# Kernel optimization log

Hardware: AMD Instinct MI355X
Metric: run time of the kernel (lower is better)

Reference implementation:

```python
import jax, jax.numpy as jnp
import numpy as np
from jax import lax

N = 100000      # number of nodes (== ninput)
E = 3200000     # number of edges per adjacency
NHID = 128
EPS = 1e-12     # torch F.normalize eps


def spmm(src, dst, w, x):
    # sparse adj @ x : out[i] = sum_{e: dst[e]==i} w[e] * x[src[e]]
    return jax.ops.segment_sum(w[:, None] * x[src], dst, num_segments=N)


def l2norm(x):
    # F.normalize(x, p=2, dim=1)
    n = jnp.sqrt(jnp.sum(x * x, axis=1, keepdims=True))
    return x / jnp.maximum(n, EPS)


def mlp(x, L1, bl1, L2, bl2, L3, bl3):
    # dropout == 0.0 -> identity; chunking is a memory optimization, same math
    h = jax.nn.relu(x @ L1 + bl1)
    h = jax.nn.relu(h @ L2 + bl2)
    return h @ L3 + bl3  # [N, 1]


def setup_inputs() -> dict:
    key = jax.random.key(0)
    ks = jax.random.split(key, 32)
    d = {}
    d["adj1_src"] = jax.random.randint(ks[0], (E,), 0, N, dtype=jnp.int32)
    d["adj1_dst"] = jax.random.randint(ks[1], (E,), 0, N, dtype=jnp.int32)
    d["adj1_w"] = jax.random.uniform(ks[2], (E,), dtype=jnp.float32)
    d["adj2_src"] = jax.random.randint(ks[3], (E,), 0, N, dtype=jnp.int32)
    d["adj2_dst"] = jax.random.randint(ks[4], (E,), 0, N, dtype=jnp.int32)
    d["adj2_w"] = jax.random.uniform(ks[5], (E,), dtype=jnp.float32)
    d["W1"] = jax.random.normal(ks[6], (N, NHID), dtype=jnp.float32) * 0.05
    d["b1"] = jnp.zeros((NHID,), jnp.float32)
    for i, k in zip(range(2, 7), ks[7:12]):
        d[f"W{i}"] = jax.random.normal(k, (NHID, NHID), dtype=jnp.float32) * (1.0 / np.sqrt(NHID))
        d[f"b{i}"] = jnp.zeros((NHID,), jnp.float32)
    d["L1"] = jax.random.normal(ks[12], (NHID, 2 * NHID), dtype=jnp.float32) * (1.0 / np.sqrt(NHID))
    d["bl1"] = jnp.zeros((2 * NHID,), jnp.float32)
    d["L2"] = jax.random.normal(ks[13], (2 * NHID, 2 * NHID), dtype=jnp.float32) * (1.0 / np.sqrt(2 * NHID))
    d["bl2"] = jnp.zeros((2 * NHID,), jnp.float32)
    d["L3"] = jax.random.normal(ks[14], (2 * NHID, 1), dtype=jnp.float32) * (1.0 / np.sqrt(2 * NHID))
    d["bl3"] = jnp.zeros((1,), jnp.float32)
    return d


def reference(adj1_src, adj1_dst, adj1_w, adj2_src, adj2_dst, adj2_w,
              W1, b1, W2, b2, W3, b3, W4, b4, W5, b5, W6, b6,
              L1, bl1, L2, bl2, L3, bl3):
    def branch(src, dst, w):
        x1 = l2norm(jax.nn.relu(spmm(src, dst, w, W1) + b1))
        x2 = l2norm(jax.nn.relu(spmm(src, dst, w, x1 @ W2) + b2))
        x3 = l2norm(jax.nn.relu(spmm(src, dst, w, x2 @ W3) + b3))
        x4 = l2norm(jax.nn.relu(spmm(src, dst, w, x3 @ W4) + b4))
        x5 = l2norm(jax.nn.relu(spmm(src, dst, w, x4 @ W5) + b5))
        x6 = jax.nn.relu(spmm(src, dst, w, x5 @ W6) + b6)
        x7 = lax.stop_gradient(x1 + x2 + x3 + x4 + x5 + x6)  # .detach()
        s = jnp.zeros((N, 1), jnp.float32)
        for xi in (x1, x2, x3, x4, x5):  # computed under torch.no_grad()
            s = s + lax.stop_gradient(mlp(xi, L1, bl1, L2, bl2, L3, bl3))
        s = s + mlp(x6, L1, bl1, L2, bl2, L3, bl3)
        s = s + mlp(x7, L1, bl1, L2, bl2, L3, bl3)
        return s / 7.0

    score1 = branch(adj1_src, adj1_dst, adj1_w)
    score2 = branch(adj2_src, adj2_dst, adj2_w)
    return score1 * score2
```

## Files before the change

### kernel.cpp

```cpp
#include <hip/hip_runtime.h>

#define NN 100000
#define NE 3200000
#define HID 128
#define NNH ((size_t)NN * HID)
#define CAPB 80

typedef __attribute__((ext_vector_type(8))) _Float16 f16x8;
typedef __attribute__((ext_vector_type(4))) _Float16 f16x4;
typedef __attribute__((ext_vector_type(4))) float f32x4;

#define SWZ(row, k) ((k) ^ (((row) & 7) << 3))

__global__ void zero_k(int* p, int n) {
    int i = blockIdx.x * 256 + threadIdx.x;
    if (i < n) p[i] = 0;
}

__global__ void scatter_bin_k(const int* __restrict__ src, const int* __restrict__ dst,
                              const float* __restrict__ w, int* __restrict__ cnt,
                              unsigned* __restrict__ ep) {
    int e = blockIdx.x * 256 + threadIdx.x;
    if (e < NE) {
        int d = dst[e];
        int pos = atomicAdd(&cnt[d], 1);
        if (pos < CAPB) {
            ushort hb = __builtin_bit_cast(ushort, (_Float16)w[e]);
            ep[(size_t)d * CAPB + pos] = ((unsigned)src[e] << 15) | (unsigned)hb;
        }
    }
}

__global__ void convT_k(const float* __restrict__ W, _Float16* __restrict__ WT, int K, int N) {
    int idx = blockIdx.x * 256 + threadIdx.x;
    if (idx < K * N) {
        int k = idx / N, n = idx % N;
        WT[n * K + k] = (_Float16)W[idx];
    }
}

__global__ void conv4_k(const float* __restrict__ A, _Float16* __restrict__ B, int n4) {
    int i = blockIdx.x * 256 + threadIdx.x;
    if (i < n4) {
        float4 v = ((const float4*)A)[i];
        f16x4 h;
        h.x = (_Float16)v.x; h.y = (_Float16)v.y; h.z = (_Float16)v.z; h.w = (_Float16)v.w;
        ((f16x4*)B)[i] = h;
    }
}

template <bool EPI>
__global__ void spmm_k(const _Float16* __restrict__ x, const int* __restrict__ cnt,
                       const unsigned* __restrict__ ep, const float* __restrict__ bias,
                       _Float16* __restrict__ outx) {
    int row = blockIdx.x * 4 + (threadIdx.x >> 6);
    int l = threadIdx.x & 63;
    int q = l >> 4, li = l & 15;
    if (row >= NN) return;
    int e0 = row * CAPB;
    int deg = cnt[row];
    if (deg > CAPB) deg = CAPB;
    int e1 = e0 + deg;
    float acc[8] = {};
#pragma unroll 4
    for (int e = e0 + q; e < e1; e += 4) {
        unsigned r = ep[e];
        int s = r >> 15;
        float w = (float)__builtin_bit_cast(_Float16, (ushort)(r & 0x7FFFu));
        f16x8 v = *(const f16x8*)(x + (size_t)s * HID + li * 8);
#pragma unroll
        for (int j = 0; j < 8; ++j) acc[j] += w * (float)v[j];
    }
#pragma unroll
    for (int j = 0; j < 8; ++j) {
        acc[j] += __shfl_xor(acc[j], 16, 64);
        acc[j] += __shfl_xor(acc[j], 32, 64);
    }
    if (EPI) {
        const float4* bp = (const float4*)(bias + li * 8);
        float4 b0 = bp[0], b1 = bp[1];
        acc[0] = fmaxf(acc[0] + b0.x, 0.f); acc[1] = fmaxf(acc[1] + b0.y, 0.f);
        acc[2] = fmaxf(acc[2] + b0.z, 0.f); acc[3] = fmaxf(acc[3] + b0.w, 0.f);
        acc[4] = fmaxf(acc[4] + b1.x, 0.f); acc[5] = fmaxf(acc[5] + b1.y, 0.f);
        acc[6] = fmaxf(acc[6] + b1.z, 0.f); acc[7] = fmaxf(acc[7] + b1.w, 0.f);
        float ss = 0.f;
#pragma unroll
        for (int j = 0; j < 8; ++j) ss += acc[j] * acc[j];
        ss += __shfl_xor(ss, 1, 64);
        ss += __shfl_xor(ss, 2, 64);
        ss += __shfl_xor(ss, 4, 64);
        ss += __shfl_xor(ss, 8, 64);
        float sc = 1.0f / fmaxf(sqrtf(ss), 1e-12f);
#pragma unroll
        for (int j = 0; j < 8; ++j) acc[j] *= sc;
    }
    if (q == 0) {
        f16x8 ho;
#pragma unroll
        for (int j = 0; j < 8; ++j) ho[j] = (_Float16)acc[j];
        *(f16x8*)(outx + (size_t)row * HID + li * 8) = ho;
    }
}

template <bool NORM>
__global__ __launch_bounds__(256) void trans_mlp_k(
    const _Float16* __restrict__ Y, const _Float16* __restrict__ WT,
    const float* __restrict__ bw, _Float16* __restrict__ Xo,
    const _Float16* __restrict__ L1T, const float* __restrict__ bl1,
    const _Float16* __restrict__ L2T, const float* __restrict__ bl2,
    const float* __restrict__ L3, const float* __restrict__ bl3,
    float* __restrict__ sacc) {
    __shared__ _Float16 Xs[64][128];
    __shared__ _Float16 H1s[64][256];
    __shared__ float red[4][64];
    int t = threadIdx.x;
    int w = t >> 6, l = t & 63;
    int g = l >> 4, li = l & 15;
    int rowBase = blockIdx.x * 64;

#pragma unroll
    for (int i = 0; i < 4; ++i) {
        int idx = t + i * 256;
        int r = idx >> 4, c8 = idx & 15;
        int gr = rowBase + r;
        f16x8 v = (gr < NN) ? *(const f16x8*)(Y + (size_t)gr * 128 + c8 * 8)
                            : (f16x8)(_Float16)0.f;
        *(f16x8*)&Xs[r][SWZ(r, c8 * 8)] = v;
    }
    __syncthreads();

    int cW = w * 32;
    f32x4 accw[4][2] = {};
#pragma unroll
    for (int ks = 0; ks < 4; ++ks) {
        int kb = ks * 32 + g * 8;
        f16x8 a[4];
#pragma unroll
        for (int mt = 0; mt < 4; ++mt) {
            int r = mt * 16 + li;
            a[mt] = *(const f16x8*)&Xs[r][SWZ(r, kb)];
        }
#pragma unroll
        for (int nt = 0; nt < 2; ++nt) {
            f16x8 b = *(const f16x8*)(WT + (size_t)(cW + nt * 16 + li) * 128 + kb);
#pragma unroll
            for (int mt = 0; mt < 4; ++mt)
                accw[mt][nt] = __builtin_amdgcn_mfma_f32_16x16x32_f16(a[mt], b, accw[mt][nt], 0, 0, 0);
        }
    }
    float vv[4][2][4];
    float b0 = bw[cW + li], b1v = bw[cW + 16 + li];
#pragma unroll
    for (int mt = 0; mt < 4; ++mt)
#pragma unroll
        for (int r4 = 0; r4 < 4; ++r4) {
            vv[mt][0][r4] = fmaxf(accw[mt][0][r4] + b0, 0.f);
            vv[mt][1][r4] = fmaxf(accw[mt][1][r4] + b1v, 0.f);
        }
    if (NORM) {
#pragma unroll
        for (int mt = 0; mt < 4; ++mt)
#pragma unroll
            for (int r4 = 0; r4 < 4; ++r4) {
                float ps = vv[mt][0][r4] * vv[mt][0][r4] + vv[mt][1][r4] * vv[mt][1][r4];
                ps += __shfl_xor(ps, 1, 64);
                ps += __shfl_xor(ps, 2, 64);
                ps += __shfl_xor(ps, 4, 64);
                ps += __shfl_xor(ps, 8, 64);
                if (li == 0) red[w][mt * 16 + g * 4 + r4] = ps;
            }
        __syncthreads();
        if (t < 64) {
            float s = red[0][t] + red[1][t] + red[2][t] + red[3][t];
            red[0][t] = 1.f / fmaxf(sqrtf(s), 1e-12f);
        }
        __syncthreads();
    } else {
        __syncthreads();
    }
#pragma unroll
    for (int mt = 0; mt < 4; ++mt)
#pragma unroll
        for (int r4 = 0; r4 < 4; ++r4) {
            int row = mt * 16 + g * 4 + r4;
            float sc = NORM ? red[0][row] : 1.f;
            _Float16 h0 = (_Float16)(vv[mt][0][r4] * sc);
            _Float16 h1 = (_Float16)(vv[mt][1][r4] * sc);
            Xs[row][SWZ(row, cW + li)] = h0;
            Xs[row][SWZ(row, cW + 16 + li)] = h1;
            int gr = rowBase + row;
            if (gr < NN) {
                Xo[(size_t)gr * 128 + cW + li] = h0;
                Xo[(size_t)gr * 128 + cW + 16 + li] = h1;
            }
        }
    __syncthreads();

    int cM = w * 64;
    f32x4 acc[4][4] = {};
#pragma unroll
    for (int ks = 0; ks < 4; ++ks) {
        int kb = ks * 32 + g * 8;
        f16x8 a[4];
#pragma unroll
        for (int mt = 0; mt < 4; ++mt) {
            int r = mt * 16 + li;
            a[mt] = *(const f16x8*)&Xs[r][SWZ(r, kb)];
        }
#pragma unroll
        for (int nt = 0; nt < 4; ++nt) {
            int n = cM + nt * 16 + li;
            f16x8 b = *(const f16x8*)(L1T + (size_t)n * 128 + kb);
#pragma unroll
            for (int mt = 0; mt < 4; ++mt)
                acc[mt][nt] = __builtin_amdgcn_mfma_f32_16x16x32_f16(a[mt], b, acc[mt][nt], 0, 0, 0);
        }
    }
#pragma unroll
    for (int nt = 0; nt < 4; ++nt) {
        int col = cM + nt * 16 + li;
        float bb = bl1[col];
#pragma unroll
        for (int mt = 0; mt < 4; ++mt)
#pragma unroll
            for (int r4 = 0; r4 < 4; ++r4) {
                int row = mt * 16 + g * 4 + r4;
                H1s[row][SWZ(row, col)] = (_Float16)fmaxf(acc[mt][nt][r4] + bb, 0.f);
            }
    }
    __syncthreads();

    f32x4 acc2[4][4] = {};
#pragma unroll
    for (int ks = 0; ks < 8; ++ks) {
        int kb = ks * 32 + g * 8;
        f16x8 a[4];
#pragma unroll
        for (int mt = 0; mt < 4; ++mt) {
            int r = mt * 16 + li;
            a[mt] = *(const f16x8*)&H1s[r][SWZ(r, kb)];
        }
#pragma unroll
        for (int nt = 0; nt < 4; ++nt) {
            int n = cM + nt * 16 + li;
            f16x8 b = *(const f16x8*)(L2T + (size_t)n * 256 + kb);
#pragma unroll
            for (int mt = 0; mt < 4; ++mt)
                acc2[mt][nt] = __builtin_amdgcn_mfma_f32_16x16x32_f16(a[mt], b, acc2[mt][nt], 0, 0, 0);
        }
    }
    float part[4][4] = {};
#pragma unroll
    for (int nt = 0; nt < 4; ++nt) {
        int col = cM + nt * 16 + li;
        float bb = bl2[col];
        float l3v = L3[col];
#pragma unroll
        for (int mt = 0; mt < 4; ++mt)
#pragma unroll
            for (int r4 = 0; r4 < 4; ++r4)
                part[mt][r4] += fmaxf(acc2[mt][nt][r4] + bb, 0.f) * l3v;
    }
#pragma unroll
    for (int mt = 0; mt < 4; ++mt)
#pragma unroll
        for (int r4 = 0; r4 < 4; ++r4) {
            float p = part[mt][r4];
            p += __shfl_xor(p, 1, 64);
            p += __shfl_xor(p, 2, 64);
            p += __shfl_xor(p, 4, 64);
            p += __shfl_xor(p, 8, 64);
            if (li == 0) red[w][mt * 16 + g * 4 + r4] = p;
        }
    __syncthreads();
    if (t < 64) {
        int gr = rowBase + t;
        if (gr < NN)
            sacc[gr] += red[0][t] + red[1][t] + red[2][t] + red[3][t] + bl3[0];
    }
}

template <bool SUM6, bool INIT>
__global__ __launch_bounds__(256) void mlp_fused_k(
    const _Float16* __restrict__ X,
    const _Float16* __restrict__ L1T, const float* __restrict__ bl1,
    const _Float16* __restrict__ L2T, const float* __restrict__ bl2,
    const float* __restrict__ L3, const float* __restrict__ bl3,
    float* __restrict__ sacc) {
    __shared__ _Float16 Xs[64][128];
    __shared__ _Float16 H1s[64][256];
    __shared__ float red[4][64];
    int t = threadIdx.x;
    int w = t >> 6, l = t & 63;
    int g = l >> 4, li = l & 15;
    int rowBase = blockIdx.x * 64;

#pragma unroll
    for (int i = 0; i < 4; ++i) {
        int idx = t + i * 256;
        int r = idx >> 4, c8 = idx & 15;
        int gr = rowBase + r;
        if (SUM6) {
            float s[8] = {};
            if (gr < NN) {
#pragma unroll
                for (int l6 = 0; l6 < 6; ++l6) {
                    f16x8 v = *(const f16x8*)(X + (size_t)l6 * NNH + (size_t)gr * HID + c8 * 8);
#pragma unroll
                    for (int j = 0; j < 8; ++j) s[j] += (float)v[j];
                }
            }
            f16x8 hv;
#pragma unroll
            for (int j = 0; j < 8; ++j) hv[j] = (_Float16)s[j];
            *(f16x8*)&Xs[r][SWZ(r, c8 * 8)] = hv;
        } else {
            f16x8 v = (gr < NN) ? *(const f16x8*)(X + (size_t)gr * HID + c8 * 8)
                                : (f16x8)(_Float16)0.f;
            *(f16x8*)&Xs[r][SWZ(r, c8 * 8)] = v;
        }
    }
    __syncthreads();

    int cM = w * 64;
    f32x4 acc[4][4] = {};
#pragma unroll
    for (int ks = 0; ks < 4; ++ks) {
        int kb = ks * 32 + g * 8;
        f16x8 a[4];
#pragma unroll
        for (int mt = 0; mt < 4; ++mt) {
            int r = mt * 16 + li;
            a[mt] = *(const f16x8*)&Xs[r][SWZ(r, kb)];
        }
#pragma unroll
        for (int nt = 0; nt < 4; ++nt) {
            int n = cM + nt * 16 + li;
            f16x8 b = *(const f16x8*)(L1T + (size_t)n * 128 + kb);
#pragma unroll
            for (int mt = 0; mt < 4; ++mt)
                acc[mt][nt] = __builtin_amdgcn_mfma_f32_16x16x32_f16(a[mt], b, acc[mt][nt], 0, 0, 0);
        }
    }
#pragma unroll
    for (int nt = 0; nt < 4; ++nt) {
        int col = cM + nt * 16 + li;
        float bb = bl1[col];
#pragma unroll
        for (int mt = 0; mt < 4; ++mt)
#pragma unroll
            for (int r4 = 0; r4 < 4; ++r4) {
                int row = mt * 16 + g * 4 + r4;
                H1s[row][SWZ(row, col)] = (_Float16)fmaxf(acc[mt][nt][r4] + bb, 0.f);
            }
    }
    __syncthreads();

    f32x4 acc2[4][4] = {};
#pragma unroll
    for (int ks = 0; ks < 8; ++ks) {
        int kb = ks * 32 + g * 8;
        f16x8 a[4];
#pragma unroll
        for (int mt = 0; mt < 4; ++mt) {
            int r = mt * 16 + li;
            a[mt] = *(const f16x8*)&H1s[r][SWZ(r, kb)];
        }
#pragma unroll
        for (int nt = 0; nt < 4; ++nt) {
            int n = cM + nt * 16 + li;
            f16x8 b = *(const f16x8*)(L2T + (size_t)n * 256 + kb);
#pragma unroll
            for (int mt = 0; mt < 4; ++mt)
                acc2[mt][nt] = __builtin_amdgcn_mfma_f32_16x16x32_f16(a[mt], b, acc2[mt][nt], 0, 0, 0);
        }
    }
    float part[4][4] = {};
#pragma unroll
    for (int nt = 0; nt < 4; ++nt) {
        int col = cM + nt * 16 + li;
        float bb = bl2[col];
        float l3v = L3[col];
#pragma unroll
        for (int mt = 0; mt < 4; ++mt)
#pragma unroll
            for (int r4 = 0; r4 < 4; ++r4)
                part[mt][r4] += fmaxf(acc2[mt][nt][r4] + bb, 0.f) * l3v;
    }
#pragma unroll
    for (int mt = 0; mt < 4; ++mt)
#pragma unroll
        for (int r4 = 0; r4 < 4; ++r4) {
            float p = part[mt][r4];
            p += __shfl_xor(p, 1, 64);
            p += __shfl_xor(p, 2, 64);
            p += __shfl_xor(p, 4, 64);
            p += __shfl_xor(p, 8, 64);
            if (li == 0) red[w][mt * 16 + g * 4 + r4] = p;
        }
    __syncthreads();
    if (t < 64) {
        int gr = rowBase + t;
        if (gr < NN) {
            float s = red[0][t] + red[1][t] + red[2][t] + red[3][t] + bl3[0];
            if (INIT) sacc[gr] = s; else sacc[gr] += s;
        }
    }
}

__global__ void score_store_k(const float* __restrict__ sacc, float* __restrict__ dst) {
    int i = blockIdx.x * 256 + threadIdx.x;
    if (i < NN) dst[i] = sacc[i] * (1.f / 7.f);
}

__global__ void final_mul_k(const float* __restrict__ sacc, const float* __restrict__ score1,
                            float* __restrict__ out) {
    int i = blockIdx.x * 256 + threadIdx.x;
    if (i < NN) out[i] = score1[i] * (sacc[i] * (1.f / 7.f));
}

extern "C" void kernel_launch(void* const* d_in, const int* in_sizes, int n_in,
                              void* d_out, int out_size, void* d_ws, size_t ws_size,
                              hipStream_t stream) {
    const int* asrc[2] = {(const int*)d_in[0], (const int*)d_in[3]};
    const int* adst[2] = {(const int*)d_in[1], (const int*)d_in[4]};
    const float* aw[2] = {(const float*)d_in[2], (const float*)d_in[5]};
    const float* W1 = (const float*)d_in[6];
    const float* b1 = (const float*)d_in[7];
    const float* Wk[5] = {(const float*)d_in[8], (const float*)d_in[10], (const float*)d_in[12],
                          (const float*)d_in[14], (const float*)d_in[16]};
    const float* bk[5] = {(const float*)d_in[9], (const float*)d_in[11], (const float*)d_in[13],
                          (const float*)d_in[15], (const float*)d_in[17]};
    const float* L1 = (const float*)d_in[18];
    const float* bl1 = (const float*)d_in[19];
    const float* L2 = (const float*)d_in[20];
    const float* bl2 = (const float*)d_in[21];
    const float* L3 = (const float*)d_in[22];
    const float* bl3 = (const float*)d_in[23];
    float* out = (float*)d_out;

    char* p = (char*)d_ws;
    _Float16* L1T = (_Float16*)p; p += 65536;
    _Float16* L2T = (_Float16*)p; p += 131072;
    _Float16* WkT = (_Float16*)p; p += 163840;
    _Float16* W1h = (_Float16*)p; p += NNH * 2;
    _Float16* tmp = (_Float16*)p; p += NNH * 2;
    _Float16* xbuf = (_Float16*)p; p += 6 * NNH * 2;
    float* sacc = (float*)p; p += (size_t)NN * 4;
    float* score1 = (float*)p; p += (size_t)NN * 4;
    unsigned* ep = (unsigned*)p; p += (size_t)NN * CAPB * 4;
    int* cnt = (int*)p; p += (size_t)NN * 4;

    const int GE = (NE + 255) / 256;
    const int GN = (NN + 255) / 256;
    const int GS = (NN + 3) / 4;
    const int GM = (NN + 63) / 64;

    convT_k<<<(128 * 256 + 255) / 256, 256, 0, stream>>>(L1, L1T, 128, 256);
    convT_k<<<(256 * 256 + 255) / 256, 256, 0, stream>>>(L2, L2T, 256, 256);
    for (int l = 0; l < 5; ++l)
        convT_k<<<(128 * 128 + 255) / 256, 256, 0, stream>>>(Wk[l], WkT + (size_t)l * 16384, 128, 128);
    conv4_k<<<(NN * HID / 4 + 255) / 256, 256, 0, stream>>>(W1, W1h, NN * HID / 4);

    for (int br = 0; br < 2; ++br) {
        zero_k<<<GN, 256, 0, stream>>>(cnt, NN);
        scatter_bin_k<<<GE, 256, 0, stream>>>(asrc[br], adst[br], aw[br], cnt, ep);

        spmm_k<true><<<GS, 256, 0, stream>>>(W1h, cnt, ep, b1, xbuf);
        mlp_fused_k<false, true><<<GM, 256, 0, stream>>>(xbuf, L1T, bl1, L2T, bl2, L3, bl3, sacc);

        for (int l = 0; l < 5; ++l) {
            spmm_k<false><<<GS, 256, 0, stream>>>(xbuf + (size_t)l * NNH, cnt, ep, b1, tmp);
            _Float16* xo = xbuf + (size_t)(l + 1) * NNH;
            if (l < 4)
                trans_mlp_k<true><<<GM, 256, 0, stream>>>(tmp, WkT + (size_t)l * 16384, bk[l], xo,
                                                          L1T, bl1, L2T, bl2, L3, bl3, sacc);
            else
                trans_mlp_k<false><<<GM, 256, 0, stream>>>(tmp, WkT + (size_t)l * 16384, bk[l], xo,
                                                           L1T, bl1, L2T, bl2, L3, bl3, sacc);
        }

        mlp_fused_k<true, false><<<GM, 256, 0, stream>>>(xbuf, L1T, bl1, L2T, bl2, L3, bl3, sacc);

        if (br == 0)
            score_store_k<<<GN, 256, 0, stream>>>(sacc, score1);
        else
            final_mul_k<<<GN, 256, 0, stream>>>(sacc, score1, out);
    }
}
```

Baseline: 2.606 ms.

## Sort per-row edges by source and process SpMM in source-row windows

Each row's edge bin is sorted by source index with a wave bitonic sort, and binary search records where each of 8 source windows begins. The SpMM kernel then walks rows window by window with block-wide barriers, so that all resident blocks gather from a similar slice of the feature matrix at the same time and get better L2/LLC reuse. This adds a sort pass, a bounds pass, extra bound loads and a barrier per window.

```diff
diff --git a/kernel.cpp b/kernel.cpp
--- a/kernel.cpp
+++ b/kernel.cpp
@@ -5,6 +5,12 @@
 #define HID 128
 #define NNH ((size_t)NN * HID)
 #define CAPB 80
+#define NWIN 8
+#define WROWS 12500
+#define PWB 2048
+#define RPW 4
+#define RPB2 16
+#define GENS 4
 
 typedef __attribute__((ext_vector_type(8))) _Float16 f16x8;
 typedef __attribute__((ext_vector_type(4))) _Float16 f16x4;
@@ -31,6 +37,77 @@
     }
 }
 
+template <bool DESC>
+__device__ inline unsigned bsort64(unsigned v, int lane) {
+#pragma unroll
+    for (int k = 2; k <= 64; k <<= 1)
+#pragma unroll
+        for (int j = k >> 1; j > 0; j >>= 1) {
+            unsigned o = __shfl_xor(v, j, 64);
+            bool keepmin = ((((lane & j) == 0) == ((lane & k) == 0))) ^ DESC;
+            unsigned mn = v < o ? v : o, mx = v < o ? o : v;
+            v = keepmin ? mn : mx;
+        }
+    return v;
+}
+
+__device__ inline unsigned bmerge64(unsigned v, int lane) {
+#pragma unroll
+    for (int j = 32; j > 0; j >>= 1) {
+        unsigned o = __shfl_xor(v, j, 64);
+        unsigned mn = v < o ? v : o, mx = v < o ? o : v;
+        v = ((lane & j) == 0) ? mn : mx;
+    }
+    return v;
+}
+
+__global__ void sort_bin_k(const int* __restrict__ cnt, unsigned* __restrict__ ep) {
+    int row = blockIdx.x * 4 + (threadIdx.x >> 6);
+    int lane = threadIdx.x & 63;
+    if (row >= NN) return;
+    int e0 = row * CAPB;
+    int deg = cnt[row];
+    if (deg > CAPB) deg = CAPB;
+    int e1 = e0 + deg;
+    if (deg <= 1) return;
+    if (deg <= 64) {
+        unsigned v = (e0 + lane < e1) ? ep[e0 + lane] : 0xFFFFFFFFu;
+        v = bsort64<false>(v, lane);
+        if (e0 + lane < e1) ep[e0 + lane] = v;
+    } else {
+        unsigned a = (e0 + lane < e1) ? ep[e0 + lane] : 0xFFFFFFFFu;
+        unsigned b = (e0 + 64 + lane < e1) ? ep[e0 + 64 + lane] : 0xFFFFFFFFu;
+        a = bsort64<false>(a, lane);
+        b = bsort64<true>(b, lane);
+        unsigned mn = a < b ? a : b, mx = a < b ? b : a;
+        a = bmerge64(mn, lane);
+        b = bmerge64(mx, lane);
+        if (e0 + lane < e1) ep[e0 + lane] = a;
+        if (e0 + 64 + lane < e1) ep[e0 + 64 + lane] = b;
+    }
+}
+
+__global__ void bounds_bin_k(const int* __restrict__ cnt, const unsigned* __restrict__ ep,
+                             int* __restrict__ bnd) {
+    int r = blockIdx.x * 256 + threadIdx.x;
+    if (r >= NN) return;
+    int e0 = r * CAPB;
+    int deg = cnt[r];
+    if (deg > CAPB) deg = CAPB;
+    int e1 = e0 + deg;
+    bnd[r] = e0;
+    bnd[(size_t)NWIN * NN + r] = e1;
+    for (int wdx = 1; wdx < NWIN; ++wdx) {
+        unsigned key = (unsigned)(wdx * WROWS) << 15;
+        int lo = e0, hi = e1;
+        while (lo < hi) {
+            int mid = (lo + hi) >> 1;
+            if (ep[mid] < key) lo = mid + 1; else hi = mid;
+        }
+        bnd[(size_t)wdx * NN + r] = lo;
+    }
+}
+
 __global__ void convT_k(const float* __restrict__ W, _Float16* __restrict__ WT, int K, int N) {
     int idx = blockIdx.x * 256 + threadIdx.x;
     if (idx < K * N) {
@@ -50,55 +127,76 @@
 }
 
 template <bool EPI>
-__global__ void spmm_k(const _Float16* __restrict__ x, const int* __restrict__ cnt,
-                       const unsigned* __restrict__ ep, const float* __restrict__ bias,
-                       _Float16* __restrict__ outx) {
-    int row = blockIdx.x * 4 + (threadIdx.x >> 6);
-    int l = threadIdx.x & 63;
+__global__ __launch_bounds__(256) void spmm_pw_k(const _Float16* __restrict__ x,
+                                                 const unsigned* __restrict__ ep,
+                                                 const int* __restrict__ bnd,
+                                                 const float* __restrict__ bias,
+                                                 _Float16* __restrict__ outx) {
+    int tid = threadIdx.x;
+    int w = tid >> 6, l = tid & 63;
     int q = l >> 4, li = l & 15;
-    if (row >= NN) return;
-    int e0 = row * CAPB;
-    int deg = cnt[row];
-    if (deg > CAPB) deg = CAPB;
-    int e1 = e0 + deg;
-    float acc[8] = {};
-#pragma unroll 4
-    for (int e = e0 + q; e < e1; e += 4) {
-        unsigned r = ep[e];
-        int s = r >> 15;
-        float w = (float)__builtin_bit_cast(_Float16, (ushort)(r & 0x7FFFu));
-        f16x8 v = *(const f16x8*)(x + (size_t)s * HID + li * 8);
-#pragma unroll
-        for (int j = 0; j < 8; ++j) acc[j] += w * (float)v[j];
-    }
-#pragma unroll
-    for (int j = 0; j < 8; ++j) {
-        acc[j] += __shfl_xor(acc[j], 16, 64);
-        acc[j] += __shfl_xor(acc[j], 32, 64);
-    }
-    if (EPI) {
-        const float4* bp = (const float4*)(bias + li * 8);
-        float4 b0 = bp[0], b1 = bp[1];
-        acc[0] = fmaxf(acc[0] + b0.x, 0.f); acc[1] = fmaxf(acc[1] + b0.y, 0.f);
-        acc[2] = fmaxf(acc[2] + b0.z, 0.f); acc[3] = fmaxf(acc[3] + b0.w, 0.f);
-        acc[4] = fmaxf(acc[4] + b1.x, 0.f); acc[5] = fmaxf(acc[5] + b1.y, 0.f);
-        acc[6] = fmaxf(acc[6] + b1.z, 0.f); acc[7] = fmaxf(acc[7] + b1.w, 0.f);
-        float ss = 0.f;
-#pragma unroll
-        for (int j = 0; j < 8; ++j) ss += acc[j] * acc[j];
-        ss += __shfl_xor(ss, 1, 64);
-        ss += __shfl_xor(ss, 2, 64);
-        ss += __shfl_xor(ss, 4, 64);
-        ss += __shfl_xor(ss, 8, 64);
-        float sc = 1.0f / fmaxf(sqrtf(ss), 1e-12f);
-#pragma unroll
-        for (int j = 0; j < 8; ++j) acc[j] *= sc;
-    }
-    if (q == 0) {
-        f16x8 ho;
-#pragma unroll
-        for (int j = 0; j < 8; ++j) ho[j] = (_Float16)acc[j];
-        *(f16x8*)(outx + (size_t)row * HID + li * 8) = ho;
+    for (int gen = 0; gen < GENS; ++gen) {
+        int rowBase = gen * (PWB * RPB2) + blockIdx.x * RPB2 + w * RPW;
+        float acc[RPW][8] = {};
+        for (int win = 0; win < NWIN; ++win) {
+            if (rowBase < NN) {
+#pragma unroll
+                for (int j = 0; j < RPW; ++j) {
+                    int r = rowBase + j;
+                    if (r >= NN) break;
+                    int b0 = bnd[(size_t)win * NN + r];
+                    int b1 = bnd[(size_t)(win + 1) * NN + r];
+                    for (int e = b0 + q; e < b1; e += 4) {
+                        unsigned rec = ep[e];
+                        float wgt = (float)__builtin_bit_cast(_Float16, (ushort)(rec & 0x7FFFu));
+                        unsigned s = rec >> 15;
+                        f16x8 v = *(const f16x8*)(x + (size_t)s * HID + li * 8);
+#pragma unroll
+                        for (int k = 0; k < 8; ++k) acc[j][k] += wgt * (float)v[k];
+                    }
+                }
+            }
+            __syncthreads();
+        }
+        if (rowBase < NN) {
+#pragma unroll
+            for (int j = 0; j < RPW; ++j) {
+                int r = rowBase + j;
+                if (r >= NN) break;
+                float a[8];
+#pragma unroll
+                for (int k = 0; k < 8; ++k) {
+                    float t = acc[j][k];
+                    t += __shfl_xor(t, 16, 64);
+                    t += __shfl_xor(t, 32, 64);
+                    a[k] = t;
+                }
+                if (EPI) {
+                    const float4* bp = (const float4*)(bias + li * 8);
+                    float4 b0 = bp[0], b1 = bp[1];
+                    a[0] = fmaxf(a[0] + b0.x, 0.f); a[1] = fmaxf(a[1] + b0.y, 0.f);
+                    a[2] = fmaxf(a[2] + b0.z, 0.f); a[3] = fmaxf(a[3] + b0.w, 0.f);
+                    a[4] = fmaxf(a[4] + b1.x, 0.f); a[5] = fmaxf(a[5] + b1.y, 0.f);
+                    a[6] = fmaxf(a[6] + b1.z, 0.f); a[7] = fmaxf(a[7] + b1.w, 0.f);
+                    float ss = 0.f;
+#pragma unroll
+                    for (int k = 0; k < 8; ++k) ss += a[k] * a[k];
+                    ss += __shfl_xor(ss, 1, 64);
+                    ss += __shfl_xor(ss, 2, 64);
+                    ss += __shfl_xor(ss, 4, 64);
+                    ss += __shfl_xor(ss, 8, 64);
+                    float sc = 1.0f / fmaxf(sqrtf(ss), 1e-12f);
+#pragma unroll
+                    for (int k = 0; k < 8; ++k) a[k] *= sc;
+                }
+                if (q == 0) {
+                    f16x8 ho;
+#pragma unroll
+                    for (int k = 0; k < 8; ++k) ho[k] = (_Float16)a[k];
+                    *(f16x8*)(outx + (size_t)r * HID + li * 8) = ho;
+                }
+            }
+        }
     }
 }
 
@@ -450,6 +548,7 @@
     float* score1 = (float*)p; p += (size_t)NN * 4;
     unsigned* ep = (unsigned*)p; p += (size_t)NN * CAPB * 4;
     int* cnt = (int*)p; p += (size_t)NN * 4;
+    int* bnd = (int*)p; p += (size_t)(NWIN + 1) * NN * 4;
 
     const int GE = (NE + 255) / 256;
     const int GN = (NN + 255) / 256;
@@ -465,12 +564,14 @@
     for (int br = 0; br < 2; ++br) {
         zero_k<<<GN, 256, 0, stream>>>(cnt, NN);
         scatter_bin_k<<<GE, 256, 0, stream>>>(asrc[br], adst[br], aw[br], cnt, ep);
-
-        spmm_k<true><<<GS, 256, 0, stream>>>(W1h, cnt, ep, b1, xbuf);
+        sort_bin_k<<<GS, 256, 0, stream>>>(cnt, ep);
+        bounds_bin_k<<<GN, 256, 0, stream>>>(cnt, ep, bnd);
+
+        spmm_pw_k<true><<<PWB, 256, 0, stream>>>(W1h, ep, bnd, b1, xbuf);
         mlp_fused_k<false, true><<<GM, 256, 0, stream>>>(xbuf, L1T, bl1, L2T, bl2, L3, bl3, sacc);
 
         for (int l = 0; l < 5; ++l) {
-            spmm_k<false><<<GS, 256, 0, stream>>>(xbuf + (size_t)l * NNH, cnt, ep, b1, tmp);
+            spmm_pw_k<false><<<PWB, 256, 0, stream>>>(xbuf + (size_t)l * NNH, ep, bnd, b1, tmp);
             _Float16* xo = xbuf + (size_t)(l + 1) * NNH;
             if (l < 4)
                 trans_mlp_k<true><<<GM, 256, 0, stream>>>(tmp, WkT + (size_t)l * 16384, bk[l], xo,
```

Result: slower. 3.814 ms (+46.4%).

## Overlap branch-2 edge binning with branch-1 SpMM blocks and drop tmp buffer

Applied to the files above, without the earlier changes.

Interleaves branch-2's scatter-binning work into the branch-1 SpMM launches: every 13th block bins a chunk of adjacency-2 edges, while the remaining blocks do SpMM rows. This hides the serial scatter kernel for the second branch behind the bandwidth-bound SpMM passes. Each branch now keeps its own binned edge list and counts. SpMM also writes directly into the output x buffer, which trans_mlp then transforms in place (restrict removed), so the separate tmp buffer goes away. The risk is that atomic contention and extra scattered traffic slow down the co-running SpMM.

```diff
diff --git a/kernel.cpp b/kernel.cpp
--- a/kernel.cpp
+++ b/kernel.cpp
@@ -5,6 +5,9 @@
 #define HID 128
 #define NNH ((size_t)NN * HID)
 #define CAPB 80
+#define SP 13
+#define FGRID 27097
+#define CHE 533504
 
 typedef __attribute__((ext_vector_type(8))) _Float16 f16x8;
 typedef __attribute__((ext_vector_type(4))) _Float16 f16x4;
@@ -50,12 +53,12 @@
 }
 
 template <bool EPI>
-__global__ void spmm_k(const _Float16* __restrict__ x, const int* __restrict__ cnt,
-                       const unsigned* __restrict__ ep, const float* __restrict__ bias,
-                       _Float16* __restrict__ outx) {
-    int row = blockIdx.x * 4 + (threadIdx.x >> 6);
+__device__ inline void spmm_rows4(const _Float16* __restrict__ x, const int* __restrict__ cnt,
+                                  const unsigned* __restrict__ ep, const float* __restrict__ bias,
+                                  _Float16* __restrict__ outx, int row0) {
     int l = threadIdx.x & 63;
     int q = l >> 4, li = l & 15;
+    int row = row0 + (threadIdx.x >> 6);
     if (row >= NN) return;
     int e0 = row * CAPB;
     int deg = cnt[row];
@@ -102,10 +105,41 @@
     }
 }
 
+template <bool EPI>
+__global__ void spmm_k(const _Float16* __restrict__ x, const int* __restrict__ cnt,
+                       const unsigned* __restrict__ ep, const float* __restrict__ bias,
+                       _Float16* __restrict__ outx) {
+    spmm_rows4<EPI>(x, cnt, ep, bias, outx, blockIdx.x * 4);
+}
+
+template <bool EPI>
+__global__ void spmm_sc_k(const _Float16* __restrict__ x, const int* __restrict__ cnt,
+                          const unsigned* __restrict__ ep, const float* __restrict__ bias,
+                          _Float16* __restrict__ outx,
+                          const int* __restrict__ src2, const int* __restrict__ dst2,
+                          const float* __restrict__ w2, int* __restrict__ cnt2,
+                          unsigned* __restrict__ ep2, int ebase) {
+    int b = blockIdx.x;
+    if (b % SP == SP - 1) {
+        int e = ebase + (b / SP) * 256 + threadIdx.x;
+        if (e < NE) {
+            int d = dst2[e];
+            int pos = atomicAdd(&cnt2[d], 1);
+            if (pos < CAPB) {
+                ushort hb = __builtin_bit_cast(ushort, (_Float16)w2[e]);
+                ep2[(size_t)d * CAPB + pos] = ((unsigned)src2[e] << 15) | (unsigned)hb;
+            }
+        }
+        return;
+    }
+    int mIdx = b - b / SP;
+    spmm_rows4<EPI>(x, cnt, ep, bias, outx, mIdx * 4);
+}
+
 template <bool NORM>
 __global__ __launch_bounds__(256) void trans_mlp_k(
-    const _Float16* __restrict__ Y, const _Float16* __restrict__ WT,
-    const float* __restrict__ bw, _Float16* __restrict__ Xo,
+    const _Float16* Y, const _Float16* __restrict__ WT,
+    const float* __restrict__ bw, _Float16* Xo,
     const _Float16* __restrict__ L1T, const float* __restrict__ bl1,
     const _Float16* __restrict__ L2T, const float* __restrict__ bl2,
     const float* __restrict__ L3, const float* __restrict__ bl3,
@@ -444,12 +478,13 @@
     _Float16* L2T = (_Float16*)p; p += 131072;
     _Float16* WkT = (_Float16*)p; p += 163840;
     _Float16* W1h = (_Float16*)p; p += NNH * 2;
-    _Float16* tmp = (_Float16*)p; p += NNH * 2;
     _Float16* xbuf = (_Float16*)p; p += 6 * NNH * 2;
     float* sacc = (float*)p; p += (size_t)NN * 4;
     float* score1 = (float*)p; p += (size_t)NN * 4;
-    unsigned* ep = (unsigned*)p; p += (size_t)NN * CAPB * 4;
-    int* cnt = (int*)p; p += (size_t)NN * 4;
+    unsigned* ep1 = (unsigned*)p; p += (size_t)NN * CAPB * 4;
+    unsigned* ep2 = (unsigned*)p; p += (size_t)NN * CAPB * 4;
+    int* cnt1 = (int*)p; p += (size_t)NN * 4;
+    int* cnt2 = (int*)p; p += (size_t)NN * 4;
 
     const int GE = (NE + 255) / 256;
     const int GN = (NN + 255) / 256;
@@ -461,30 +496,42 @@
     for (int l = 0; l < 5; ++l)
         convT_k<<<(128 * 128 + 255) / 256, 256, 0, stream>>>(Wk[l], WkT + (size_t)l * 16384, 128, 128);
     conv4_k<<<(NN * HID / 4 + 255) / 256, 256, 0, stream>>>(W1, W1h, NN * HID / 4);
-
-    for (int br = 0; br < 2; ++br) {
-        zero_k<<<GN, 256, 0, stream>>>(cnt, NN);
-        scatter_bin_k<<<GE, 256, 0, stream>>>(asrc[br], adst[br], aw[br], cnt, ep);
-
-        spmm_k<true><<<GS, 256, 0, stream>>>(W1h, cnt, ep, b1, xbuf);
-        mlp_fused_k<false, true><<<GM, 256, 0, stream>>>(xbuf, L1T, bl1, L2T, bl2, L3, bl3, sacc);
-
-        for (int l = 0; l < 5; ++l) {
-            spmm_k<false><<<GS, 256, 0, stream>>>(xbuf + (size_t)l * NNH, cnt, ep, b1, tmp);
-            _Float16* xo = xbuf + (size_t)(l + 1) * NNH;
-            if (l < 4)
-                trans_mlp_k<true><<<GM, 256, 0, stream>>>(tmp, WkT + (size_t)l * 16384, bk[l], xo,
-                                                          L1T, bl1, L2T, bl2, L3, bl3, sacc);
-            else
-                trans_mlp_k<false><<<GM, 256, 0, stream>>>(tmp, WkT + (size_t)l * 16384, bk[l], xo,
-                                                           L1T, bl1, L2T, bl2, L3, bl3, sacc);
-        }
-
-        mlp_fused_k<true, false><<<GM, 256, 0, stream>>>(xbuf, L1T, bl1, L2T, bl2, L3, bl3, sacc);
-
-        if (br == 0)
-            score_store_k<<<GN, 256, 0, stream>>>(sacc, score1);
+    zero_k<<<GN, 256, 0, stream>>>(cnt1, NN);
+    zero_k<<<GN, 256, 0, stream>>>(cnt2, NN);
+
+    scatter_bin_k<<<GE, 256, 0, stream>>>(asrc[0], adst[0], aw[0], cnt1, ep1);
+
+    spmm_sc_k<true><<<FGRID, 256, 0, stream>>>(W1h, cnt1, ep1, b1, xbuf,
+                                               asrc[1], adst[1], aw[1], cnt2, ep2, 0);
+    mlp_fused_k<false, true><<<GM, 256, 0, stream>>>(xbuf, L1T, bl1, L2T, bl2, L3, bl3, sacc);
+
+    for (int l = 0; l < 5; ++l) {
+        _Float16* xo = xbuf + (size_t)(l + 1) * NNH;
+        spmm_sc_k<false><<<FGRID, 256, 0, stream>>>(xbuf + (size_t)l * NNH, cnt1, ep1, b1, xo,
+                                                    asrc[1], adst[1], aw[1], cnt2, ep2,
+                                                    (l + 1) * CHE);
+        if (l < 4)
+            trans_mlp_k<true><<<GM, 256, 0, stream>>>(xo, WkT + (size_t)l * 16384, bk[l], xo,
+                                                      L1T, bl1, L2T, bl2, L3, bl3, sacc);
         else
-            final_mul_k<<<GN, 256, 0, stream>>>(sacc, score1, out);
-    }
-}
+            trans_mlp_k<false><<<GM, 256, 0, stream>>>(xo, WkT + (size_t)l * 16384, bk[l], xo,
+                                                       L1T, bl1, L2T, bl2, L3, bl3, sacc);
+    }
+    mlp_fused_k<true, false><<<GM, 256, 0, stream>>>(xbuf, L1T, bl1, L2T, bl2, L3, bl3, sacc);
+    score_store_k<<<GN, 256, 0, stream>>>(sacc, score1);
+
+    spmm_k<true><<<GS, 256, 0, stream>>>(W1h, cnt2, ep2, b1, xbuf);
+    mlp_fused_k<false, true><<<GM, 256, 0, stream>>>(xbuf, L1T, bl1, L2T, bl2, L3, bl3, sacc);
+    for (int l = 0; l < 5; ++l) {
+        _Float16* xo = xbuf + (size_t)(l + 1) * NNH;
+        spmm_k<false><<<GS, 256, 0, stream>>>(xbuf + (size_t)l * NNH, cnt2, ep2, b1, xo);
+        if (l < 4)
+            trans_mlp_k<true><<<GM, 256, 0, stream>>>(xo, WkT + (size_t)l * 16384, bk[l], xo,
+                                                      L1T, bl1, L2T, bl2, L3, bl3, sacc);
+        else
+            trans_mlp_k<false><<<GM, 256, 0, stream>>>(xo, WkT + (size_t)l * 16384, bk[l], xo,
+                                                       L1T, bl1, L2T, bl2, L3, bl3, sacc);
+    }
+    mlp_fused_k<true, false><<<GM, 256, 0, stream>>>(xbuf, L1T, bl1, L2T, bl2, L3, bl3, sacc);
+    final_mul_k<<<GN, 256, 0, stream>>>(sacc, score1, out);
+}
```

Measured after the change: 2.482 ms. 4.8% less time.
